# Kernel tuning notes

Hardware: AMD Instinct MI355X
Metric: run time of the kernel (lower is better)

## Reference

```python
import jax, jax.numpy as jnp
import numpy as np

N_NODES = 8192
N_EDGES = 65536
NB = 10            # number_of_basis
MID = 32           # middle_layer_size
MAX_R = 10.0       # max_radius
NZ, NM = 48, 16    # z / mol embedding sizes -> 64x0e node input
IN_S = NZ + NM     # 64 scalars
H_S, H_V = 32, 8   # hidden irreps 32x0e + 8x1o (dim 56)
O_S = 16           # output irreps 16x0e
W0N = IN_S * H_S + IN_S * H_V                                  # 2560
W1N = H_S*H_S + H_V*H_S + H_S*H_V + H_V*H_V + H_V*H_V          # 1664
W2N = H_S*O_S + H_V*O_S                                        # 640
H_DIM = H_S + 3 * H_V                                          # 56


def _fcnet(e, W1, W2):
    # e3nn FullyConnectedNet([NB, MID, numel], silu): fan-in normalized linears
    h = jax.nn.silu(e @ W1 / np.sqrt(W1.shape[0]))
    return h @ W2 / np.sqrt(W2.shape[0])


def _ln(x, g, b):
    m = jnp.mean(x, -1, keepdims=True)
    v = jnp.var(x, -1, keepdims=True)
    return (x - m) * jax.lax.rsqrt(v + 1e-5) * g + b


def _sus(t):
    # smooth compact-support bump helper: exp(-1/t) for t>0 else 0
    return jnp.where(t > 0, jnp.exp(-1.0 / jnp.where(t > 0, t, 1.0)), 0.0)


def _forward(pos, Ez, Em,
             b0_W1, b0_W2, b0_g, b0_b,
             b1_W1, b1_W2, b1_g, b1_b,
             b2_W1, b2_W2, b2_g, b2_b,
             z, mol_id, edge_src, edge_dst):
    N = pos.shape[0]
    E = edge_src.shape[0]
    avg = E / N  # avg_num_neighbors (static)

    # node embedding: 64x0e
    x = jnp.concatenate([Ez[z], Em[mol_id]], axis=-1)          # [N, 64]

    vec = pos[edge_dst] - pos[edge_src]                        # [E, 3]
    length = jnp.linalg.norm(vec, axis=1)                      # [E]

    # soft_one_hot_linspace(basis='smooth_finite', cutoff=True) * sqrt(NB)
    vals = jnp.linspace(0.0, MAX_R, NB + 2)[1:-1]
    step = MAX_R / (NB + 1)
    u = (length[:, None] - vals) / step
    emb = (1.14136 * np.exp(2.0)) * _sus(u + 1.0) * _sus(1.0 - u)
    emb = emb * np.sqrt(NB)                                    # [E, NB]

    # spherical harmonics lmax=1, normalize=True, 'component' norm
    nrm = vec / jnp.maximum(length, 1e-9)[:, None]
    sh_v = np.sqrt(3.0) * nrm                                  # [E, 3]  (l=1; l=0 comp == 1)

    # ---- interaction block 0: 64x0e -> 32x0e + 8x1o ----
    w = _fcnet(emb, b0_W1, b0_W2)                              # [E, 2560]
    w00 = w[:, :IN_S * H_S].reshape(E, IN_S, H_S)
    w01 = w[:, IN_S * H_S:].reshape(E, IN_S, H_V)
    xe = x[edge_src]                                           # [E, 64]
    es = jnp.einsum('eu,euw->ew', xe, w00) / np.sqrt(IN_S)
    ev = jnp.einsum('eu,euw,ei->ewi', xe, w01, sh_v) / np.sqrt(IN_S)
    msg = jnp.concatenate([es, ev.reshape(E, 3 * H_V)], -1)    # [E, 56]
    x = _ln(jax.ops.segment_sum(msg, edge_dst, num_segments=N) / np.sqrt(avg), b0_g, b0_b)

    # ---- interaction block 1: 32x0e+8x1o -> 32x0e+8x1o ----
    w = _fcnet(emb, b1_W1, b1_W2)                              # [E, 1664]
    o = 0
    w_ss  = w[:, o:o + H_S*H_S].reshape(E, H_S, H_S); o += H_S*H_S
    w_vvs = w[:, o:o + H_V*H_S].reshape(E, H_V, H_S); o += H_V*H_S
    w_sv  = w[:, o:o + H_S*H_V].reshape(E, H_S, H_V); o += H_S*H_V
    w_vs  = w[:, o:o + H_V*H_V].reshape(E, H_V, H_V); o += H_V*H_V
    w_vvv = w[:, o:o + H_V*H_V].reshape(E, H_V, H_V)
    xs = x[:, :H_S][edge_src]                                  # [E, 32]
    xv = x[:, H_S:].reshape(N, H_V, 3)[edge_src]               # [E, 8, 3]
    dot = jnp.einsum('eui,ei->eu', xv, sh_v) / np.sqrt(3.0)    # 1o x 1o -> 0e CG
    crs = jnp.cross(xv, sh_v[:, None, :]) / np.sqrt(2.0)       # 1o x 1o -> 1o CG
    es = (jnp.einsum('eu,euw->ew', xs, w_ss) / np.sqrt(H_S)
          + jnp.einsum('eu,euw->ew', dot, w_vvs) / np.sqrt(H_V)) / np.sqrt(2.0)
    ev = (jnp.einsum('eu,euw,ei->ewi', xs, w_sv, sh_v) / np.sqrt(H_S)
          + jnp.einsum('eui,euw->ewi', xv, w_vs) / np.sqrt(H_V)
          + jnp.einsum('eui,euw->ewi', crs, w_vvv) / np.sqrt(H_V)) / np.sqrt(3.0)
    msg = jnp.concatenate([es, ev.reshape(E, 3 * H_V)], -1)
    x = _ln(jax.ops.segment_sum(msg, edge_dst, num_segments=N) / np.sqrt(avg), b1_g, b1_b)

    # ---- interaction block 2: 32x0e+8x1o -> 16x0e ----
    w = _fcnet(emb, b2_W1, b2_W2)                              # [E, 640]
    w_ss  = w[:, :H_S * O_S].reshape(E, H_S, O_S)
    w_vvs = w[:, H_S * O_S:].reshape(E, H_V, O_S)
    xs = x[:, :H_S][edge_src]
    xv = x[:, H_S:].reshape(N, H_V, 3)[edge_src]
    dot = jnp.einsum('eui,ei->eu', xv, sh_v) / np.sqrt(3.0)
    es = (jnp.einsum('eu,euw->ew', xs, w_ss) / np.sqrt(H_S)
          + jnp.einsum('eu,euw->ew', dot, w_vvs) / np.sqrt(H_V)) / np.sqrt(2.0)
    x = _ln(jax.ops.segment_sum(es, edge_dst, num_segments=N) / np.sqrt(avg), b2_g, b2_b)
    return x                                                   # [N, 16]


def setup_inputs():
    key = jax.random.key(0)
    ks = jax.random.split(key, 16)
    edge_src = jax.random.randint(ks[3], (N_EDGES,), 0, N_NODES)
    # exclude self-loops (radius_graph never returns them)
    edge_dst = (edge_src + 1 + jax.random.randint(ks[4], (N_EDGES,), 0, N_NODES - 1)) % N_NODES
    return {
        'pos': jax.random.uniform(ks[0], (N_NODES, 3), jnp.float32) * 8.0,
        'z': jax.random.randint(ks[1], (N_NODES,), 0, 100),
        'mol_id': jax.random.randint(ks[2], (N_NODES,), 0, 2),
        'edge_src': edge_src,
        'edge_dst': edge_dst,
        'Ez': jax.random.normal(ks[5], (100, NZ), jnp.float32),
        'Em': jax.random.normal(ks[6], (2, NM), jnp.float32),
        'b0_W1': jax.random.normal(ks[7], (NB, MID), jnp.float32),
        'b0_W2': jax.random.normal(ks[8], (MID, W0N), jnp.float32),
        'b0_g': jnp.ones((H_DIM,), jnp.float32),
        'b0_b': jnp.zeros((H_DIM,), jnp.float32),
        'b1_W1': jax.random.normal(ks[9], (NB, MID), jnp.float32),
        'b1_W2': jax.random.normal(ks[10], (MID, W1N), jnp.float32),
        'b1_g': jnp.ones((H_DIM,), jnp.float32),
        'b1_b': jnp.zeros((H_DIM,), jnp.float32),
        'b2_W1': jax.random.normal(ks[11], (NB, MID), jnp.float32),
        'b2_W2': jax.random.normal(ks[12], (MID, W2N), jnp.float32),
        'b2_g': jnp.ones((O_S,), jnp.float32),
        'b2_b': jnp.zeros((O_S,), jnp.float32),
    }


def reference(pos, z, mol_id, edge_src, edge_dst, Ez, Em,
              b0_W1, b0_W2, b0_g, b0_b,
              b1_W1, b1_W2, b1_g, b1_b,
              b2_W1, b2_W2, b2_g, b2_b):
    return _forward(pos, Ez, Em,
                    b0_W1, b0_W2, b0_g, b0_b,
                    b1_W1, b1_W2, b1_g, b1_b,
                    b2_W1, b2_W2, b2_g, b2_b,
                    z, mol_id, edge_src, edge_dst)
```

## Files before the change

### kernel.cpp

```cpp
#include <hip/hip_runtime.h>

#define NNODES 8192
#define NEDGES 65536

#define K_PACK   0.02209708691f
#define K_P1SV   0.01804219593f
#define K_VVS    0.04419417382f
#define K_VS     0.03608439182f
#define K_VVV    0.02551551815f
#define K_DOT    0.57735026919f
#define K_PRELN  0.35355339059f
#define C_EMB    8.4335730689f

typedef unsigned int uint32;
typedef unsigned short ushort16;
typedef __attribute__((ext_vector_type(8))) short short8;
typedef __attribute__((ext_vector_type(4))) float floatx4;

__device__ __forceinline__ float siluf(float x) { return x / (1.0f + __expf(-x)); }
__device__ __forceinline__ float susf(float t) { return t > 0.0f ? __expf(-1.0f / t) : 0.0f; }
__device__ __forceinline__ ushort16 f2bf(float f) {
  uint32 u = __float_as_uint(f);
  return (ushort16)((u + 0x7fffu + ((u >> 16) & 1u)) >> 16);
}
__device__ __forceinline__ float bflo(uint32 v) { return __uint_as_float(v << 16); }
__device__ __forceinline__ float bfhi(uint32 v) { return __uint_as_float(v & 0xffff0000u); }
__device__ __forceinline__ float bfs(ushort16 v) { return __uint_as_float((uint32)v << 16); }

__global__ __launch_bounds__(256) void k_prep(
    const float* __restrict__ pos, const int* __restrict__ z, const int* __restrict__ mol,
    const int* __restrict__ esrc, const int* __restrict__ edst,
    const float* __restrict__ Ez, const float* __restrict__ Em,
    const float* __restrict__ W10, const float* __restrict__ W11, const float* __restrict__ W12,
    const float* __restrict__ W20, const float* __restrict__ W21, const float* __restrict__ W22,
    int* __restrict__ combo, ushort16* __restrict__ X0cb, float* __restrict__ sh,
    ushort16* __restrict__ h0b, ushort16* __restrict__ h1b, ushort16* __restrict__ h2b,
    ushort16* __restrict__ Bp0, ushort16* __restrict__ Bp1, ushort16* __restrict__ Bp2,
    ushort16* __restrict__ Bpw1, ushort16* __restrict__ Bpw2,
    int* __restrict__ deg, int* __restrict__ eidx) {
  __shared__ float Wl[320];
  int b = blockIdx.x;
  if (b < 768) {
    int which = b >> 8;
    int e = ((b & 255) << 8) + threadIdx.x;
    const float* W = (which == 0) ? W10 : (which == 1) ? W11 : W12;
    for (int i = threadIdx.x; i < 320; i += 256) Wl[i] = W[i];
    __syncthreads();
    int s = esrc[e], d = edst[e];
    float vx = pos[d * 3 + 0] - pos[s * 3 + 0];
    float vy = pos[d * 3 + 1] - pos[s * 3 + 1];
    float vz = pos[d * 3 + 2] - pos[s * 3 + 2];
    float len = sqrtf(vx * vx + vy * vy + vz * vz);
    if (which == 0) {
      int p = atomicAdd(&deg[d], 1);
      if (p < 64) eidx[(size_t)d * 64 + p] = e;
      float inv = 1.7320508076f / fmaxf(len, 1e-9f);
      sh[e * 3 + 0] = vx * inv; sh[e * 3 + 1] = vy * inv; sh[e * 3 + 2] = vz * inv;
    }
    float emb[10];
#pragma unroll
    for (int k = 0; k < 10; ++k) {
      float u = len * 1.1f - (float)(k + 1);
      emb[k] = C_EMB * susf(u + 1.0f) * susf(1.0f - u);
    }
    float H[32];
#pragma unroll
    for (int m = 0; m < 32; ++m) {
      float t = 0.f;
#pragma unroll
      for (int k = 0; k < 10; ++k) t += emb[k] * Wl[k * 32 + m];
      H[m] = siluf(t);
    }
    ushort16* hb = (which == 0) ? h0b : (which == 1) ? h1b : h2b;
    uint32* hp = (uint32*)(hb + (size_t)e * 32);
#pragma unroll
    for (int m = 0; m < 16; ++m)
      hp[m] = (uint32)f2bf(H[2 * m]) | ((uint32)f2bf(H[2 * m + 1]) << 16);
    return;
  }
  int idx = (b - 768) * 256 + threadIdx.x;
  if (idx < NNODES) { combo[idx] = z[idx] * 2 + mol[idx]; return; }
  idx -= NNODES;
  if (idx < 16384) {
    int c = idx >> 6, j = idx & 63;
    float v = 0.f;
    if (c < 200) {
      int zz = c >> 1, mm = c & 1;
      v = (j < 48) ? Ez[zz * 48 + j] : Em[mm * 16 + (j - 48)];
    }
    X0cb[idx] = f2bf(v);
    return;
  }
  idx -= 16384;
  if (idx < 81920) {
    int tile = idx >> 10; int r = idx & 1023;
    int kh = r >> 9; int rr = r & 511;
    int lane = rr >> 3, j = rr & 7;
    int k = kh * 32 + (lane >> 4) * 8 + j;
    int n = tile * 16 + (lane & 15);
    int c = n >> 5, m = n & 31;
    int col = (c < 32) ? (k * 32 + c) : (2048 + k * 8 + (c - 32));
    Bp0[idx] = f2bf(W20[m * 2560 + col] * K_PACK);
    return;
  }
  idx -= 81920;
  if (idx < 40960) {
    int tile = idx >> 9; int rr = idx & 511;
    int lane = rr >> 3, j = rr & 7;
    int k = (lane >> 4) * 8 + j;
    int n = tile * 16 + (lane & 15);
    int c = n >> 5, m = n & 31;
    float v = (c < 32) ? W21[m * 1664 + k * 32 + c] * K_PACK
                       : W21[m * 1664 + 1280 + k * 8 + (c - 32)] * K_P1SV;
    Bp1[idx] = f2bf(v);
    return;
  }
  idx -= 40960;
  if (idx < 16384) {
    int tile = idx >> 9; int rr = idx & 511;
    int lane = rr >> 3, j = rr & 7;
    int k = (lane >> 4) * 8 + j;
    int n = tile * 16 + (lane & 15);
    int c = n >> 5, m = n & 31;
    Bp2[idx] = f2bf(W22[m * 640 + k * 16 + c] * K_PACK);
    return;
  }
  idx -= 16384;
  if (idx < 12288) {
    int tile = idx >> 9; int rr = idx & 511;
    int lane = rr >> 3, j = rr & 7;
    int m = (lane >> 4) * 8 + j;
    int n = tile * 16 + (lane & 15);
    float v;
    if (n < 256) {
      int c = n >> 3, u = n & 7;
      v = W21[m * 1664 + 1024 + u * 32 + c] * K_VVS;
    } else if (n < 320) {
      int vo = (n - 256) >> 3, u = n & 7;
      v = W21[m * 1664 + 1536 + u * 8 + vo] * K_VS;
    } else {
      int vo = (n - 320) >> 3, u = n & 7;
      v = W21[m * 1664 + 1600 + u * 8 + vo] * K_VVV;
    }
    Bpw1[idx] = f2bf(v);
    return;
  }
  idx -= 12288;
  {
    int tile = idx >> 9; int rr = idx & 511;
    int lane = rr >> 3, j = rr & 7;
    int m = (lane >> 4) * 8 + j;
    int n = tile * 16 + (lane & 15);
    int c = n >> 3, u = n & 7;
    Bpw2[idx] = f2bf(W22[m * 640 + 512 + u * 16 + c] * K_VVS);
  }
}

__device__ __forceinline__ void gemm_tile(
    const ushort16* __restrict__ A, const ushort16* __restrict__ Bp, ushort16* __restrict__ C,
    int N, int K, int bx, int by, int wave, int lane) {
  int m0 = bx * 64 + wave * 16;
  int n0 = by * 64;
  int row = lane & 15, q = lane >> 4;
  int nkh = K >> 5;
  floatx4 acc[4];
  floatx4 zero = {0.f, 0.f, 0.f, 0.f};
#pragma unroll
  for (int t = 0; t < 4; ++t) acc[t] = zero;
  for (int kh = 0; kh < nkh; ++kh) {
    short8 a = *reinterpret_cast<const short8*>(A + (size_t)(m0 + row) * K + kh * 32 + q * 8);
#pragma unroll
    for (int t = 0; t < 4; ++t) {
      int T = (n0 >> 4) + t;
      short8 b = *reinterpret_cast<const short8*>(Bp + ((size_t)T * nkh + kh) * 512 + lane * 8);
      acc[t] = __builtin_amdgcn_mfma_f32_16x16x32_bf16(a, b, acc[t], 0, 0, 0);
    }
  }
  int colb = n0 + row;
#pragma unroll
  for (int t = 0; t < 4; ++t)
#pragma unroll
    for (int r = 0; r < 4; ++r)
      C[(size_t)(m0 + q * 4 + r) * N + colb + t * 16] = f2bf(acc[t][r]);
}

__global__ __launch_bounds__(256) void k_gemm_mfma(
    const ushort16* __restrict__ A, const ushort16* __restrict__ Bp, ushort16* __restrict__ C,
    int N, int K) {
  gemm_tile(A, Bp, C, N, K, blockIdx.x, blockIdx.y, threadIdx.x >> 6, threadIdx.x & 63);
}

__global__ __launch_bounds__(256) void k_gather0(
    const int* __restrict__ deg, const int* __restrict__ eidx,
    const int* __restrict__ combo, const int* __restrict__ esrc,
    const float* __restrict__ sh, const ushort16* __restrict__ hb,
    const ushort16* __restrict__ Pb,
    const float* __restrict__ g, const float* __restrict__ b,
    ushort16* __restrict__ xsb, float* __restrict__ xvf) {
  int n = __builtin_amdgcn_readfirstlane(blockIdx.x * 4 + (threadIdx.x >> 6));
  int lane = threadIdx.x & 63;
  int row = lane & 15, q = lane >> 4;
  int cnt = deg[n]; if (cnt > 64) cnt = 64;
  const int* ep = eidx + (size_t)n * 64;
  int lv = lane - 32;
  int vq = (lv >= 0) ? ((lv / 3 > 7) ? 7 : lv / 3) : 0;
  int vi = (lv >= 0) ? (lv - (lv / 3) * 3) : 0;
  int c2 = 32 + row; if (c2 > 39) c2 = 39;
  floatx4 zero = {0.f, 0.f, 0.f, 0.f};
  float v = 0.f;
  int e_n = 0, s_n = 0, rp_n = 0;
  if (cnt > 0) {
    e_n = __builtin_amdgcn_readfirstlane(ep[0]);
    s_n = __builtin_amdgcn_readfirstlane(esrc[e_n]);
    rp_n = __builtin_amdgcn_readfirstlane(combo[s_n]);
  }
  for (int j = 0; j < cnt; ++j) {
    int e = e_n, rp = rp_n;
    if (j + 1 < cnt) {
      e_n = __builtin_amdgcn_readfirstlane(ep[j + 1]);
      s_n = __builtin_amdgcn_readfirstlane(esrc[e_n]);
      rp_n = __builtin_amdgcn_readfirstlane(combo[s_n]);
    }
    float sh0 = sh[e * 3 + 0], sh1 = sh[e * 3 + 1], sh2 = sh[e * 3 + 2];
    short8 af = *reinterpret_cast<const short8*>(hb + (size_t)e * 32 + q * 8);
    const ushort16* Pr = Pb + (size_t)rp * 1280;
    short8 bf0 = *reinterpret_cast<const short8*>(Pr + row * 32 + q * 8);
    short8 bf1 = *reinterpret_cast<const short8*>(Pr + (16 + row) * 32 + q * 8);
    short8 bf2 = *reinterpret_cast<const short8*>(Pr + c2 * 32 + q * 8);
    floatx4 p0 = __builtin_amdgcn_mfma_f32_16x16x32_bf16(af, bf0, zero, 0, 0, 0);
    floatx4 p1 = __builtin_amdgcn_mfma_f32_16x16x32_bf16(af, bf1, zero, 0, 0, 0);
    floatx4 p2 = __builtin_amdgcn_mfma_f32_16x16x32_bf16(af, bf2, zero, 0, 0, 0);
    float pv2 = __shfl(p2[0], vq, 64);
    float pdot = (lane < 16) ? p0[0] : (lane < 32) ? p1[0] : pv2;
    float mult = (lane < 32) ? 1.0f : ((vi == 0) ? sh0 : (vi == 1) ? sh1 : sh2);
    v += pdot * mult;
  }
  v *= K_PRELN;
  if (lane >= 56) v = 0.f;
  float sm = v, sq = v * v;
#pragma unroll
  for (int off = 32; off > 0; off >>= 1) {
    sm += __shfl_xor(sm, off, 64);
    sq += __shfl_xor(sq, off, 64);
  }
  float invD = 1.0f / 56.0f;
  float mean = sm * invD;
  float var = sq * invD - mean * mean;
  float rs = rsqrtf(var + 1e-5f);
  float r = (v - mean) * rs * g[lane < 56 ? lane : 0] + b[lane < 56 ? lane : 0];
  if (lane < 32) xsb[(size_t)n * 32 + lane] = f2bf(r);
  else if (lane < 56) xvf[(size_t)n * 24 + lane - 32] = r;
}

__global__ __launch_bounds__(256) void k_msg1f(
    const int* __restrict__ esrc, const float* __restrict__ sh, const ushort16* __restrict__ hb,
    const ushort16* __restrict__ Pb, const float* __restrict__ xv,
    const ushort16* __restrict__ Bpw, ushort16* __restrict__ msg) {
  __shared__ ushort16 Wlds[16][392];
  int w = threadIdx.x >> 6, lane = threadIdx.x & 63;
  int e0 = __builtin_amdgcn_readfirstlane(blockIdx.x * 16);
  int row = lane & 15, q = lane >> 4;
  int sK[4];
  float shK[4][3];
  short8 afK[4];
#pragma unroll
  for (int k = 0; k < 4; ++k) {
    int e = e0 + w * 4 + k;
    sK[k] = __builtin_amdgcn_readfirstlane(esrc[e]);
    shK[k][0] = sh[e * 3 + 0]; shK[k][1] = sh[e * 3 + 1]; shK[k][2] = sh[e * 3 + 2];
    afK[k] = *reinterpret_cast<const short8*>(hb + (size_t)e * 32 + q * 8);
  }
  short8 a1 = *reinterpret_cast<const short8*>(hb + (size_t)(e0 + row) * 32 + q * 8);
  floatx4 zero = {0.f, 0.f, 0.f, 0.f};
#pragma unroll
  for (int t6 = 0; t6 < 6; ++t6) {
    int T = w * 6 + t6;
    short8 b1 = *reinterpret_cast<const short8*>(Bpw + (size_t)T * 512 + lane * 8);
    floatx4 acc = __builtin_amdgcn_mfma_f32_16x16x32_bf16(a1, b1, zero, 0, 0, 0);
#pragma unroll
    for (int r = 0; r < 4; ++r)
      Wlds[q * 4 + r][T * 16 + row] = f2bf(acc[r]);
  }
  __syncthreads();
  int lv = lane - 32;
  int vq = (lv >= 0) ? ((lv / 3 > 7) ? 7 : lv / 3) : 0;
  int vi = (lv >= 0) ? (lv - (lv / 3) * 3) : 0;
  int c2 = 32 + row; if (c2 > 39) c2 = 39;
#pragma unroll
  for (int k = 0; k < 4; ++k) {
    int e = e0 + w * 4 + k;
    int s = sK[k];
    float sh0 = shK[k][0], sh1 = shK[k][1], sh2 = shK[k][2];
    const ushort16* Pr = Pb + (size_t)s * 1280;
    short8 bf0 = *reinterpret_cast<const short8*>(Pr + row * 32 + q * 8);
    short8 bf1 = *reinterpret_cast<const short8*>(Pr + (16 + row) * 32 + q * 8);
    short8 bf2 = *reinterpret_cast<const short8*>(Pr + c2 * 32 + q * 8);
    const float* xr = xv + (size_t)s * 24;
    const ushort16* wp = &Wlds[w * 4 + k][0];
    float vterm, mult;
    if (lane < 32) {
      mult = 1.0f;
      uint4 wv = *reinterpret_cast<const uint4*>(wp + lane * 8);
      float ww[8] = {bflo(wv.x), bfhi(wv.x), bflo(wv.y), bfhi(wv.y),
                     bflo(wv.z), bfhi(wv.z), bflo(wv.w), bfhi(wv.w)};
      float a0 = 0.f, a1s = 0.f, a2 = 0.f;
#pragma unroll
      for (int u = 0; u < 8; ++u) {
        a0 += xr[u * 3 + 0] * ww[u];
        a1s += xr[u * 3 + 1] * ww[u];
        a2 += xr[u * 3 + 2] * ww[u];
      }
      vterm = K_DOT * (a0 * sh0 + a1s * sh1 + a2 * sh2);
    } else {
      float shi = (vi == 0) ? sh0 : (vi == 1) ? sh1 : sh2;
      float s1 = (vi == 0) ? sh1 : (vi == 1) ? sh2 : sh0;
      float s2 = (vi == 0) ? sh2 : (vi == 1) ? sh0 : sh1;
      mult = shi;
      uint4 wvs = *reinterpret_cast<const uint4*>(wp + 256 + vq * 8);
      uint4 wvv = *reinterpret_cast<const uint4*>(wp + 320 + vq * 8);
      float vsw[8] = {bflo(wvs.x), bfhi(wvs.x), bflo(wvs.y), bfhi(wvs.y),
                      bflo(wvs.z), bfhi(wvs.z), bflo(wvs.w), bfhi(wvs.w)};
      float vvw[8] = {bflo(wvv.x), bfhi(wvv.x), bflo(wvv.y), bfhi(wvv.y),
                      bflo(wvv.z), bfhi(wvv.z), bflo(wvv.w), bfhi(wvv.w)};
      float b0 = 0.f, b1 = 0.f, b2 = 0.f;
#pragma unroll
      for (int u = 0; u < 8; ++u) {
        float xu0 = xr[u * 3], xu1 = xr[u * 3 + 1], xu2 = xr[u * 3 + 2];
        float xui = (vi == 0) ? xu0 : (vi == 1) ? xu1 : xu2;
        float xi1 = (vi == 0) ? xu1 : (vi == 1) ? xu2 : xu0;
        float xi2 = (vi == 0) ? xu2 : (vi == 1) ? xu0 : xu1;
        b0 += xui * vsw[u];
        b1 += xi1 * vvw[u];
        b2 += xi2 * vvw[u];
      }
      vterm = b0 + s2 * b1 - s1 * b2;
    }
    floatx4 p0 = __builtin_amdgcn_mfma_f32_16x16x32_bf16(afK[k], bf0, zero, 0, 0, 0);
    floatx4 p1 = __builtin_amdgcn_mfma_f32_16x16x32_bf16(afK[k], bf1, zero, 0, 0, 0);
    floatx4 p2 = __builtin_amdgcn_mfma_f32_16x16x32_bf16(afK[k], bf2, zero, 0, 0, 0);
    float pv2 = __shfl(p2[0], vq, 64);
    float pdot = (lane < 16) ? p0[0] : (lane < 32) ? p1[0] : pv2;
    if (lane < 56) msg[(size_t)e * 56 + lane] = f2bf(pdot * mult + vterm);
  }
}

__global__ __launch_bounds__(256) void k_msg2f(
    const int* __restrict__ esrc, const float* __restrict__ sh, const ushort16* __restrict__ hb,
    const ushort16* __restrict__ Pb, const float* __restrict__ xv,
    const ushort16* __restrict__ Bpw, ushort16* __restrict__ msg) {
  __shared__ ushort16 Wlds[16][136];
  int w = threadIdx.x >> 6, lane = threadIdx.x & 63;
  int e0 = __builtin_amdgcn_readfirstlane(blockIdx.x * 16);
  int row = lane & 15, q = lane >> 4;
  int sK[4];
  float shK[4][3];
  short8 afK[4];
#pragma unroll
  for (int k = 0; k < 4; ++k) {
    int e = e0 + w * 4 + k;
    sK[k] = __builtin_amdgcn_readfirstlane(esrc[e]);
    shK[k][0] = sh[e * 3 + 0]; shK[k][1] = sh[e * 3 + 1]; shK[k][2] = sh[e * 3 + 2];
    afK[k] = *reinterpret_cast<const short8*>(hb + (size_t)e * 32 + q * 8);
  }
  short8 a1 = *reinterpret_cast<const short8*>(hb + (size_t)(e0 + row) * 32 + q * 8);
  floatx4 zero = {0.f, 0.f, 0.f, 0.f};
#pragma unroll
  for (int t2 = 0; t2 < 2; ++t2) {
    int T = w * 2 + t2;
    short8 b1 = *reinterpret_cast<const short8*>(Bpw + (size_t)T * 512 + lane * 8);
    floatx4 acc = __builtin_amdgcn_mfma_f32_16x16x32_bf16(a1, b1, zero, 0, 0, 0);
#pragma unroll
    for (int r = 0; r < 4; ++r)
      Wlds[q * 4 + r][T * 16 + row] = f2bf(acc[r]);
  }
  __syncthreads();
  int cch = lane & 15;
#pragma unroll
  for (int k = 0; k < 4; ++k) {
    int e = e0 + w * 4 + k;
    int s = sK[k];
    float sh0 = shK[k][0], sh1 = shK[k][1], sh2 = shK[k][2];
    short8 bf = *reinterpret_cast<const short8*>(Pb + (size_t)s * 512 + row * 32 + q * 8);
    const float* xr = xv + (size_t)s * 24;
    uint4 wv = *reinterpret_cast<const uint4*>(&Wlds[w * 4 + k][0] + cch * 8);
    float ww[8] = {bflo(wv.x), bfhi(wv.x), bflo(wv.y), bfhi(wv.y),
                   bflo(wv.z), bfhi(wv.z), bflo(wv.w), bfhi(wv.w)};
    float a0 = 0.f, a1s = 0.f, a2 = 0.f;
#pragma unroll
    for (int u = 0; u < 8; ++u) {
      a0 += xr[u * 3 + 0] * ww[u];
      a1s += xr[u * 3 + 1] * ww[u];
      a2 += xr[u * 3 + 2] * ww[u];
    }
    float vterm = K_DOT * (a0 * sh0 + a1s * sh1 + a2 * sh2);
    floatx4 p0 = __builtin_amdgcn_mfma_f32_16x16x32_bf16(afK[k], bf, zero, 0, 0, 0);
    if (lane < 16) msg[(size_t)e * 16 + lane] = f2bf(p0[0] + vterm);
  }
}

__global__ __launch_bounds__(256) void k_gather_ln(
    const int* __restrict__ deg, const int* __restrict__ eidx,
    const ushort16* __restrict__ msg, int D,
    const float* __restrict__ g, const float* __restrict__ b,
    ushort16* __restrict__ xsb, float* __restrict__ xvf, float* __restrict__ outf) {
  int n = __builtin_amdgcn_readfirstlane(blockIdx.x * 4 + (threadIdx.x >> 6));
  int lane = threadIdx.x & 63;
  int cnt = deg[n]; if (cnt > 64) cnt = 64;
  const int* ep = eidx + (size_t)n * 64;
  float v = 0.f;
  int e_n = (cnt > 0) ? __builtin_amdgcn_readfirstlane(ep[0]) : 0;
  for (int j = 0; j < cnt; ++j) {
    int e = e_n;
    if (j + 1 < cnt) e_n = __builtin_amdgcn_readfirstlane(ep[j + 1]);
    if (lane < D) v += bfs(msg[(size_t)e * D + lane]);
  }
  v *= K_PRELN;
  if (lane >= D) v = 0.f;
  float sm = v, sq = v * v;
#pragma unroll
  for (int off = 32; off > 0; off >>= 1) {
    sm += __shfl_xor(sm, off, 64);
    sq += __shfl_xor(sq, off, 64);
  }
  float invD = 1.0f / (float)D;
  float mean = sm * invD;
  float var = sq * invD - mean * mean;
  float rs = rsqrtf(var + 1e-5f);
  float r = (v - mean) * rs * g[lane < D ? lane : 0] + b[lane < D ? lane : 0];
  if (outf) {
    if (lane < D) outf[(size_t)n * D + lane] = r;
  } else {
    if (lane < 32) xsb[(size_t)n * 32 + lane] = f2bf(r);
    else if (lane < 56) xvf[(size_t)n * 24 + lane - 32] = r;
  }
}

extern "C" void kernel_launch(void* const* d_in, const int* in_sizes, int n_in,
                              void* d_out, int out_size, void* d_ws, size_t ws_size,
                              hipStream_t stream) {
  const float* pos = (const float*)d_in[0];
  const int* z = (const int*)d_in[1];
  const int* mol = (const int*)d_in[2];
  const int* esrc = (const int*)d_in[3];
  const int* edst = (const int*)d_in[4];
  const float* Ez = (const float*)d_in[5];
  const float* Em = (const float*)d_in[6];
  const float* b0W1 = (const float*)d_in[7];
  const float* b0W2 = (const float*)d_in[8];
  const float* b0g = (const float*)d_in[9];
  const float* b0b = (const float*)d_in[10];
  const float* b1W1 = (const float*)d_in[11];
  const float* b1W2 = (const float*)d_in[12];
  const float* b1g = (const float*)d_in[13];
  const float* b1b = (const float*)d_in[14];
  const float* b2W1 = (const float*)d_in[15];
  const float* b2W2 = (const float*)d_in[16];
  const float* b2g = (const float*)d_in[17];
  const float* b2b = (const float*)d_in[18];
  float* out = (float*)d_out;

  float* ws = (float*)d_ws;
  size_t o = 0;
  int* combo = (int*)(ws + o); o += NNODES;
  int* deg = (int*)(ws + o); o += NNODES;
  int* eidx = (int*)(ws + o); o += (size_t)NNODES * 64;
  ushort16* X0cb = (ushort16*)(ws + o); o += 8192;
  ushort16* xs1b = (ushort16*)(ws + o); o += 131072;
  float* xv1 = ws + o; o += (size_t)NNODES * 24;
  ushort16* h0b = (ushort16*)(ws + o); o += (size_t)NEDGES * 16;
  ushort16* h1b = (ushort16*)(ws + o); o += (size_t)NEDGES * 16;
  ushort16* h2b = (ushort16*)(ws + o); o += (size_t)NEDGES * 16;
  float* shb = ws + o; o += (size_t)NEDGES * 3;
  ushort16* Bp0 = (ushort16*)(ws + o); o += 40960;
  ushort16* Bp1 = (ushort16*)(ws + o); o += 20480;
  ushort16* Bp2 = (ushort16*)(ws + o); o += 8192;
  ushort16* Bpw1 = (ushort16*)(ws + o); o += 6144;
  ushort16* Bpw2 = (ushort16*)(ws + o); o += 2048;
  ushort16* P12 = (ushort16*)(ws + o); o += (size_t)NNODES * 640;
  ushort16* msgb = (ushort16*)(ws + o); o += (size_t)NEDGES * 28;

  ushort16* P0c = P12;
  ushort16* xs2b = xs1b;
  float* xv2 = xv1;
  ushort16* msg16 = msgb;

  hipMemsetAsync(deg, 0, NNODES * sizeof(int), stream);

  k_prep<<<1472, 256, 0, stream>>>(pos, z, mol, esrc, edst, Ez, Em,
                                   b0W1, b1W1, b2W1, b0W2, b1W2, b2W2,
                                   combo, X0cb, shb, h0b, h1b, h2b,
                                   Bp0, Bp1, Bp2, Bpw1, Bpw2, deg, eidx);

  k_gemm_mfma<<<dim3(4, 20), 256, 0, stream>>>(X0cb, Bp0, P0c, 1280, 64);
  k_gather0<<<2048, 256, 0, stream>>>(deg, eidx, combo, esrc, shb, h0b, P0c,
                                      b0g, b0b, xs1b, xv1);

  k_gemm_mfma<<<dim3(128, 20), 256, 0, stream>>>(xs1b, Bp1, P12, 1280, 32);
  k_msg1f<<<4096, 256, 0, stream>>>(esrc, shb, h1b, P12, xv1, Bpw1, msgb);
  k_gather_ln<<<2048, 256, 0, stream>>>(deg, eidx, msgb, 56, b1g, b1b, xs2b, xv2, nullptr);

  k_gemm_mfma<<<dim3(128, 8), 256, 0, stream>>>(xs2b, Bp2, P12, 512, 32);
  k_msg2f<<<4096, 256, 0, stream>>>(esrc, shb, h2b, P12, xv2, Bpw2, msg16);
  k_gather_ln<<<2048, 256, 0, stream>>>(deg, eidx, msg16, 16, b2g, b2b, nullptr, nullptr, out);
}
```

Measured before the change: 203.4 us.

## Process message edges in source-sorted order via counting-sort permutation

Counts out-degree per source node during prep, computes a prefix sum in an extra block fused into the first GEMM launch, and builds a source-sorted edge permutation inside gather0. The message kernels then process edges in that order, with a block-index swizzle, so consecutive edges share the same source rows of the per-node projection tables and improve cache reuse. The cost is extra atomics, a serial single-block scan, and an indirection load per edge. Messages are still written by the original edge index, so the results stay the same.

```diff
diff --git a/kernel.cpp b/kernel.cpp
--- a/kernel.cpp
+++ b/kernel.cpp
@@ -37,7 +37,7 @@
     ushort16* __restrict__ h0b, ushort16* __restrict__ h1b, ushort16* __restrict__ h2b,
     ushort16* __restrict__ Bp0, ushort16* __restrict__ Bp1, ushort16* __restrict__ Bp2,
     ushort16* __restrict__ Bpw1, ushort16* __restrict__ Bpw2,
-    int* __restrict__ deg, int* __restrict__ eidx) {
+    int* __restrict__ deg, int* __restrict__ deg_s, int* __restrict__ eidx) {
   __shared__ float Wl[320];
   int b = blockIdx.x;
   if (b < 768) {
@@ -54,6 +54,7 @@
     if (which == 0) {
       int p = atomicAdd(&deg[d], 1);
       if (p < 64) eidx[(size_t)d * 64 + p] = e;
+      atomicAdd(&deg_s[s], 1);
       float inv = 1.7320508076f / fmaxf(len, 1e-9f);
       sh[e * 3 + 0] = vx * inv; sh[e * 3 + 1] = vy * inv; sh[e * 3 + 2] = vz * inv;
     }
@@ -190,13 +191,43 @@
   gemm_tile(A, Bp, C, N, K, blockIdx.x, blockIdx.y, threadIdx.x >> 6, threadIdx.x & 63);
 }
 
+__global__ __launch_bounds__(256) void k_gemm_scan(
+    const ushort16* __restrict__ A, const ushort16* __restrict__ Bp, ushort16* __restrict__ C,
+    const int* __restrict__ deg_s, int* __restrict__ rowptr_s) {
+  __shared__ int sums[256];
+  int b = blockIdx.x;
+  if (b < 80) {
+    gemm_tile(A, Bp, C, 1280, 64, b & 3, b >> 2, threadIdx.x >> 6, threadIdx.x & 63);
+    return;
+  }
+  int t = threadIdx.x;
+  int base = t * 32;
+  int local[32];
+  int s = 0;
+#pragma unroll
+  for (int i = 0; i < 32; ++i) { local[i] = s; s += deg_s[base + i]; }
+  sums[t] = s;
+  __syncthreads();
+  for (int off = 1; off < 256; off <<= 1) {
+    int v = (t >= off) ? sums[t - off] : 0;
+    __syncthreads();
+    sums[t] += v;
+    __syncthreads();
+  }
+  int prev = (t == 0) ? 0 : sums[t - 1];
+#pragma unroll
+  for (int i = 0; i < 32; ++i) rowptr_s[base + i] = prev + local[i];
+  if (t == 255) rowptr_s[NNODES] = sums[255];
+}
+
 __global__ __launch_bounds__(256) void k_gather0(
     const int* __restrict__ deg, const int* __restrict__ eidx,
     const int* __restrict__ combo, const int* __restrict__ esrc,
     const float* __restrict__ sh, const ushort16* __restrict__ hb,
     const ushort16* __restrict__ Pb,
     const float* __restrict__ g, const float* __restrict__ b,
-    ushort16* __restrict__ xsb, float* __restrict__ xvf) {
+    ushort16* __restrict__ xsb, float* __restrict__ xvf,
+    const int* __restrict__ rowptr_s, int* __restrict__ fill_s, int* __restrict__ eperm) {
   int n = __builtin_amdgcn_readfirstlane(blockIdx.x * 4 + (threadIdx.x >> 6));
   int lane = threadIdx.x & 63;
   int row = lane & 15, q = lane >> 4;
@@ -215,11 +246,15 @@
     rp_n = __builtin_amdgcn_readfirstlane(combo[s_n]);
   }
   for (int j = 0; j < cnt; ++j) {
-    int e = e_n, rp = rp_n;
+    int e = e_n, s = s_n, rp = rp_n;
     if (j + 1 < cnt) {
       e_n = __builtin_amdgcn_readfirstlane(ep[j + 1]);
       s_n = __builtin_amdgcn_readfirstlane(esrc[e_n]);
       rp_n = __builtin_amdgcn_readfirstlane(combo[s_n]);
+    }
+    if (lane == 0) {
+      int p = atomicAdd(&fill_s[s], 1);
+      eperm[rowptr_s[s] + p] = e;
     }
     float sh0 = sh[e * 3 + 0], sh1 = sh[e * 3 + 1], sh2 = sh[e * 3 + 2];
     short8 af = *reinterpret_cast<const short8*>(hb + (size_t)e * 32 + q * 8);
@@ -253,24 +288,29 @@
 }
 
 __global__ __launch_bounds__(256) void k_msg1f(
-    const int* __restrict__ esrc, const float* __restrict__ sh, const ushort16* __restrict__ hb,
+    const int* __restrict__ eperm, const int* __restrict__ esrc,
+    const float* __restrict__ sh, const ushort16* __restrict__ hb,
     const ushort16* __restrict__ Pb, const float* __restrict__ xv,
     const ushort16* __restrict__ Bpw, ushort16* __restrict__ msg) {
   __shared__ ushort16 Wlds[16][392];
   int w = threadIdx.x >> 6, lane = threadIdx.x & 63;
-  int e0 = __builtin_amdgcn_readfirstlane(blockIdx.x * 16);
+  int bid = blockIdx.x;
+  int swz = (bid & 7) * 512 + (bid >> 3);
+  int e0 = __builtin_amdgcn_readfirstlane(swz * 16);
   int row = lane & 15, q = lane >> 4;
-  int sK[4];
+  int eK[4], sK[4];
   float shK[4][3];
   short8 afK[4];
 #pragma unroll
   for (int k = 0; k < 4; ++k) {
-    int e = e0 + w * 4 + k;
+    int e = __builtin_amdgcn_readfirstlane(eperm[e0 + w * 4 + k]);
+    eK[k] = e;
     sK[k] = __builtin_amdgcn_readfirstlane(esrc[e]);
     shK[k][0] = sh[e * 3 + 0]; shK[k][1] = sh[e * 3 + 1]; shK[k][2] = sh[e * 3 + 2];
     afK[k] = *reinterpret_cast<const short8*>(hb + (size_t)e * 32 + q * 8);
   }
-  short8 a1 = *reinterpret_cast<const short8*>(hb + (size_t)(e0 + row) * 32 + q * 8);
+  int er = eperm[e0 + row];
+  short8 a1 = *reinterpret_cast<const short8*>(hb + (size_t)er * 32 + q * 8);
   floatx4 zero = {0.f, 0.f, 0.f, 0.f};
 #pragma unroll
   for (int t6 = 0; t6 < 6; ++t6) {
@@ -288,7 +328,7 @@
   int c2 = 32 + row; if (c2 > 39) c2 = 39;
 #pragma unroll
   for (int k = 0; k < 4; ++k) {
-    int e = e0 + w * 4 + k;
+    int e = eK[k];
     int s = sK[k];
     float sh0 = shK[k][0], sh1 = shK[k][1], sh2 = shK[k][2];
     const ushort16* Pr = Pb + (size_t)s * 1280;
@@ -345,24 +385,29 @@
 }
 
 __global__ __launch_bounds__(256) void k_msg2f(
-    const int* __restrict__ esrc, const float* __restrict__ sh, const ushort16* __restrict__ hb,
+    const int* __restrict__ eperm, const int* __restrict__ esrc,
+    const float* __restrict__ sh, const ushort16* __restrict__ hb,
     const ushort16* __restrict__ Pb, const float* __restrict__ xv,
     const ushort16* __restrict__ Bpw, ushort16* __restrict__ msg) {
   __shared__ ushort16 Wlds[16][136];
   int w = threadIdx.x >> 6, lane = threadIdx.x & 63;
-  int e0 = __builtin_amdgcn_readfirstlane(blockIdx.x * 16);
+  int bid = blockIdx.x;
+  int swz = (bid & 7) * 512 + (bid >> 3);
+  int e0 = __builtin_amdgcn_readfirstlane(swz * 16);
   int row = lane & 15, q = lane >> 4;
-  int sK[4];
+  int eK[4], sK[4];
   float shK[4][3];
   short8 afK[4];
 #pragma unroll
   for (int k = 0; k < 4; ++k) {
-    int e = e0 + w * 4 + k;
+    int e = __builtin_amdgcn_readfirstlane(eperm[e0 + w * 4 + k]);
+    eK[k] = e;
     sK[k] = __builtin_amdgcn_readfirstlane(esrc[e]);
     shK[k][0] = sh[e * 3 + 0]; shK[k][1] = sh[e * 3 + 1]; shK[k][2] = sh[e * 3 + 2];
     afK[k] = *reinterpret_cast<const short8*>(hb + (size_t)e * 32 + q * 8);
   }
-  short8 a1 = *reinterpret_cast<const short8*>(hb + (size_t)(e0 + row) * 32 + q * 8);
+  int er = eperm[e0 + row];
+  short8 a1 = *reinterpret_cast<const short8*>(hb + (size_t)er * 32 + q * 8);
   floatx4 zero = {0.f, 0.f, 0.f, 0.f};
 #pragma unroll
   for (int t2 = 0; t2 < 2; ++t2) {
@@ -377,7 +422,7 @@
   int cch = lane & 15;
 #pragma unroll
   for (int k = 0; k < 4; ++k) {
-    int e = e0 + w * 4 + k;
+    int e = eK[k];
     int s = sK[k];
     float sh0 = shK[k][0], sh1 = shK[k][1], sh2 = shK[k][2];
     short8 bf = *reinterpret_cast<const short8*>(Pb + (size_t)s * 512 + row * 32 + q * 8);
@@ -463,6 +508,10 @@
   size_t o = 0;
   int* combo = (int*)(ws + o); o += NNODES;
   int* deg = (int*)(ws + o); o += NNODES;
+  int* deg_s = (int*)(ws + o); o += NNODES;
+  int* fill_s = (int*)(ws + o); o += NNODES;
+  int* rowptr_s = (int*)(ws + o); o += NNODES + 8;
+  int* eperm = (int*)(ws + o); o += NEDGES;
   int* eidx = (int*)(ws + o); o += (size_t)NNODES * 64;
   ushort16* X0cb = (ushort16*)(ws + o); o += 8192;
   ushort16* xs1b = (ushort16*)(ws + o); o += 131072;
@@ -484,22 +533,22 @@
   float* xv2 = xv1;
   ushort16* msg16 = msgb;
 
-  hipMemsetAsync(deg, 0, NNODES * sizeof(int), stream);
+  hipMemsetAsync(deg, 0, 3 * NNODES * sizeof(int), stream);
 
   k_prep<<<1472, 256, 0, stream>>>(pos, z, mol, esrc, edst, Ez, Em,
                                    b0W1, b1W1, b2W1, b0W2, b1W2, b2W2,
                                    combo, X0cb, shb, h0b, h1b, h2b,
-                                   Bp0, Bp1, Bp2, Bpw1, Bpw2, deg, eidx);
-
-  k_gemm_mfma<<<dim3(4, 20), 256, 0, stream>>>(X0cb, Bp0, P0c, 1280, 64);
+                                   Bp0, Bp1, Bp2, Bpw1, Bpw2, deg, deg_s, eidx);
+
+  k_gemm_scan<<<81, 256, 0, stream>>>(X0cb, Bp0, P0c, deg_s, rowptr_s);
   k_gather0<<<2048, 256, 0, stream>>>(deg, eidx, combo, esrc, shb, h0b, P0c,
-                                      b0g, b0b, xs1b, xv1);
+                                      b0g, b0b, xs1b, xv1, rowptr_s, fill_s, eperm);
 
   k_gemm_mfma<<<dim3(128, 20), 256, 0, stream>>>(xs1b, Bp1, P12, 1280, 32);
-  k_msg1f<<<4096, 256, 0, stream>>>(esrc, shb, h1b, P12, xv1, Bpw1, msgb);
+  k_msg1f<<<4096, 256, 0, stream>>>(eperm, esrc, shb, h1b, P12, xv1, Bpw1, msgb);
   k_gather_ln<<<2048, 256, 0, stream>>>(deg, eidx, msgb, 56, b1g, b1b, xs2b, xv2, nullptr);
 
   k_gemm_mfma<<<dim3(128, 8), 256, 0, stream>>>(xs2b, Bp2, P12, 512, 32);
-  k_msg2f<<<4096, 256, 0, stream>>>(esrc, shb, h2b, P12, xv2, Bpw2, msg16);
+  k_msg2f<<<4096, 256, 0, stream>>>(eperm, esrc, shb, h2b, P12, xv2, Bpw2, msg16);
   k_gather_ln<<<2048, 256, 0, stream>>>(deg, eidx, msg16, 16, b2g, b2b, nullptr, nullptr, out);
 }
```

New measurement: 208.4 us. 2.5% more time.
